# Kernel tuning notes

Hardware: AMD Instinct MI355X
Metric: run time of the kernel (lower is better)

The kernel has to match this reference:

```python
import jax, jax.numpy as jnp
import numpy as np

H = 16  # num_heads

def setup_inputs() -> dict:
    key = jax.random.key(0)
    ks = jax.random.split(key, 5)
    C = 1024
    x = jax.random.normal(ks[0], (4, 2048, C), dtype=jnp.float32)
    # torch nn.Linear params: weight (out, in), bias (out,)
    qkv_w = jax.random.normal(ks[1], (3 * C, C), dtype=jnp.float32) * (C ** -0.5)
    qkv_b = jnp.zeros((3 * C,), dtype=jnp.float32)
    proj_w = jax.random.normal(ks[2], (C, C), dtype=jnp.float32) * (C ** -0.5)
    proj_b = jnp.zeros((C,), dtype=jnp.float32)
    return {"x": x, "qkv_w": qkv_w, "qkv_b": qkv_b, "proj_w": proj_w, "proj_b": proj_b}

def reference(x, qkv_w, qkv_b, proj_w, proj_b):
    B, T, C = x.shape
    hd = C // H
    scale = hd ** -0.5
    qkv = x @ qkv_w.T + qkv_b                      # [B,T,3C]
    qkv = qkv.reshape(B, T, 3, H, hd)
    q, k, v = jnp.moveaxis(qkv, 2, 0)              # each [B,T,H,hd]
    q = q.transpose(0, 2, 1, 3)                    # [B,H,T,hd]
    k = k.transpose(0, 2, 1, 3)
    v = v.transpose(0, 2, 1, 3)
    attn = jnp.einsum('bhqd,bhkd->bhqk', q, k) * scale
    attn = jax.nn.softmax(attn, axis=-1)           # dropout is identity at eval
    out = jnp.einsum('bhqk,bhkd->bhqd', attn, v)   # [B,H,T,hd]
    out = out.transpose(0, 2, 1, 3).reshape(B, T, C)
    return out @ proj_w.T + proj_b
```

## Files before the change

kernel.cpp:

```cpp
#include <hip/hip_runtime.h>


typedef _Float16 f16x8 __attribute__((ext_vector_type(8)));
typedef _Float16 f16x4 __attribute__((ext_vector_type(4)));
typedef __fp16 h16x2 __attribute__((ext_vector_type(2)));
typedef float f32x4 __attribute__((ext_vector_type(4)));

__device__ __forceinline__ uint4 cvt8h(const float* p) {
    float4 a = *(const float4*)p, b = *(const float4*)(p + 4);
    union { _Float16 h[8]; uint4 u; } t;
    t.h[0] = (_Float16)a.x; t.h[1] = (_Float16)a.y;
    t.h[2] = (_Float16)a.z; t.h[3] = (_Float16)a.w;
    t.h[4] = (_Float16)b.x; t.h[5] = (_Float16)b.y;
    t.h[6] = (_Float16)b.z; t.h[7] = (_Float16)b.w;
    return t.u;
}

__device__ __forceinline__ void dma16(const _Float16* g, _Float16* l) {
    __builtin_amdgcn_global_load_lds(
        (const __attribute__((address_space(1))) unsigned int*)g,
        (__attribute__((address_space(3))) unsigned int*)l, 16, 0, 0);
}

__global__ __launch_bounds__(256) void cvt_fp16(
    const float* __restrict__ x, const float* __restrict__ w1,
    const float* __restrict__ w2,
    _Float16* __restrict__ xh, _Float16* __restrict__ w1h,
    _Float16* __restrict__ w2h)
{
    const int g = blockIdx.x * 256 + threadIdx.x;
    const float* src; _Float16* dst; int off;
    if (g < 1048576)      { src = x;  dst = xh;  off = g; }
    else if (g < 1441792) { src = w1; dst = w1h; off = g - 1048576; }
    else                  { src = w2; dst = w2h; off = g - 1441792; }
    const size_t e = (size_t)off * 8;
    *(uint4*)(dst + e) = cvt8h(src + e);
}

__global__ __launch_bounds__(256) void qkv_gemm(
    const _Float16* __restrict__ X, const _Float16* __restrict__ W,
    const float* __restrict__ Bias,
    _Float16* __restrict__ qws, _Float16* __restrict__ kws,
    _Float16* __restrict__ vtws)
{
    __shared__ _Float16 sA[128 * 32];
    __shared__ _Float16 sB[128 * 32];
    const int tid = threadIdx.x;
    const int wave = tid >> 6, lane = tid & 63;
    const int wm = (wave >> 1) * 64, wn = (wave & 1) * 64;
    const int lr = lane & 15, lq = lane >> 4;
    const int m0 = blockIdx.y * 128, n0 = blockIdx.x * 128;
    const int s = n0 >> 10;

    const int drow = wave * 16 + (lane >> 2);
    const int dcol = (lane & 3) * 8;
    _Float16* ldsA = sA + wave * 512;
    _Float16* ldsB = sB + wave * 512;
    const _Float16* gA = X + (size_t)(m0 + drow) * 1024 + dcol;
    const _Float16* gB = W + (size_t)(n0 + drow) * 1024 + dcol;

    f32x4 acc[4][4] = {};

    for (int k0 = 0; k0 < 1024; k0 += 32) {
        dma16(gA + k0, ldsA);
        dma16(gA + (size_t)64 * 1024 + k0, ldsA + 2048);
        dma16(gB + k0, ldsB);
        dma16(gB + (size_t)64 * 1024 + k0, ldsB + 2048);
        __syncthreads();
        f16x8 af[4], bf[4];
        #pragma unroll
        for (int i = 0; i < 4; ++i) {
            af[i] = *(const f16x8*)&sA[(wm + i * 16 + lr) * 32 + lq * 8];
            bf[i] = *(const f16x8*)&sB[(wn + i * 16 + lr) * 32 + lq * 8];
        }
        #pragma unroll
        for (int mi = 0; mi < 4; ++mi)
            #pragma unroll
            for (int ni = 0; ni < 4; ++ni)
                acc[mi][ni] = __builtin_amdgcn_mfma_f32_16x16x32_f16(
                    af[mi], bf[ni], acc[mi][ni], 0, 0, 0);
        __syncthreads();
    }

    #pragma unroll
    for (int mi = 0; mi < 4; ++mi) {
        #pragma unroll
        for (int ni = 0; ni < 4; ++ni) {
            const int n = n0 + wn + ni * 16 + lr;
            const float bv = Bias[n];
            const int h = (n >> 6) & 15, d = n & 63;
            const int mbase = m0 + wm + mi * 16 + lq * 4;
            const int b = mbase >> 11, t0 = mbase & 2047;
            const int bh = b * 16 + h;
            if (s == 0) {
                #pragma unroll
                for (int r = 0; r < 4; ++r)
                    qws[((size_t)bh * 2048 + t0 + r) * 64 + d] =
                        (_Float16)((acc[mi][ni][r] + bv) * 0.18033688f);
            } else if (s == 1) {
                #pragma unroll
                for (int r = 0; r < 4; ++r)
                    kws[((size_t)bh * 2048 + t0 + r) * 64 + d] =
                        (_Float16)(acc[mi][ni][r] + bv);
            } else {
                f16x4 pk;
                #pragma unroll
                for (int r = 0; r < 4; ++r) pk[r] = (_Float16)(acc[mi][ni][r] + bv);
                *(f16x4*)&vtws[((size_t)bh * 64 + d) * 2048 + t0] = pk;
            }
        }
    }
}

__global__ __launch_bounds__(256, 4) void attn_kernel(
    const _Float16* __restrict__ qws,
    const _Float16* __restrict__ kws,
    const _Float16* __restrict__ vtws,
    _Float16* __restrict__ ows)
{
    __shared__ _Float16 sK[64][72];
    __shared__ _Float16 sV[64][72];
    const int bid = blockIdx.x;
    const int bh = (bid & 7) * 8 + ((bid >> 3) & 7);
    const int qb = bid >> 6;
    const int tid = threadIdx.x, wave = tid >> 6, lane = tid & 63;
    const int lr = lane & 15, lq = lane >> 4;

    const _Float16* gq = qws + ((size_t)bh * 2048 + qb * 128) * 64;
    f16x8 aQ[2][2];
    #pragma unroll
    for (int mb = 0; mb < 2; ++mb)
        #pragma unroll
        for (int ks = 0; ks < 2; ++ks)
            aQ[mb][ks] = *(const f16x8*)&gq[(wave * 32 + mb * 16 + lr) * 64 + ks * 32 + lq * 8];

    f32x4 o[2][4] = {};
    float l_loc[2] = {};

    for (int kt = 0; kt < 32; ++kt) {
        const _Float16* gk = kws + ((size_t)bh * 2048 + kt * 64) * 64;
        const _Float16* gv = vtws + (size_t)bh * 64 * 2048 + kt * 64;
        __syncthreads();
        for (int i = tid; i < 512; i += 256) {
            const int row = i >> 3, c = (i & 7) * 8;
            *(uint4*)&sK[row][c] = *(const uint4*)&gk[row * 64 + c];
            *(uint4*)&sV[row][c] = *(const uint4*)&gv[(size_t)row * 2048 + c];
        }
        __syncthreads();

        f16x8 bK[2][4];
        #pragma unroll
        for (int ks = 0; ks < 2; ++ks)
            #pragma unroll
            for (int nb = 0; nb < 4; ++nb)
                bK[ks][nb] = *(const f16x8*)&sK[nb * 16 + lr][ks * 32 + lq * 8];
        f32x4 st[4][2] = {};
        __builtin_amdgcn_s_setprio(1);
        #pragma unroll
        for (int nb = 0; nb < 4; ++nb)
            #pragma unroll
            for (int mb = 0; mb < 2; ++mb) {
                st[nb][mb] = __builtin_amdgcn_mfma_f32_16x16x32_f16(
                    bK[0][nb], aQ[mb][0], st[nb][mb], 0, 0, 0);
                st[nb][mb] = __builtin_amdgcn_mfma_f32_16x16x32_f16(
                    bK[1][nb], aQ[mb][1], st[nb][mb], 0, 0, 0);
            }
        __builtin_amdgcn_s_setprio(0);

        f16x4 pB16[4][2];
        #pragma unroll
        for (int nb = 0; nb < 4; ++nb)
            #pragma unroll
            for (int mb = 0; mb < 2; ++mb) {
                float e0 = exp2f(st[nb][mb][0]);
                float e1 = exp2f(st[nb][mb][1]);
                float e2 = exp2f(st[nb][mb][2]);
                float e3 = exp2f(st[nb][mb][3]);
                l_loc[mb] += (e0 + e1) + (e2 + e3);
                union { h16x2 v2[2]; f16x4 v4; } u;
                u.v2[0] = __builtin_amdgcn_cvt_pkrtz(e0, e1);
                u.v2[1] = __builtin_amdgcn_cvt_pkrtz(e2, e3);
                pB16[nb][mb] = u.v4;
            }

        __builtin_amdgcn_s_setprio(1);
        #pragma unroll
        for (int nb = 0; nb < 4; ++nb) {
            f16x4 vA16[4];
            #pragma unroll
            for (int db = 0; db < 4; ++db)
                vA16[db] = *(const f16x4*)&sV[db * 16 + lr][nb * 16 + lq * 4];
            #pragma unroll
            for (int mb = 0; mb < 2; ++mb)
                #pragma unroll
                for (int db = 0; db < 4; ++db)
                    o[mb][db] = __builtin_amdgcn_mfma_f32_16x16x16f16(
                        vA16[db], pB16[nb][mb], o[mb][db], 0, 0, 0);
        }
        __builtin_amdgcn_s_setprio(0);
    }

    const int b = bh >> 4, h = bh & 15;
    #pragma unroll
    for (int mb = 0; mb < 2; ++mb) {
        float l = l_loc[mb];
        l += __shfl_xor(l, 16, 64);
        l += __shfl_xor(l, 32, 64);
        const float linv = 1.0f / l;
        const int t = qb * 128 + wave * 32 + mb * 16 + lr;
        #pragma unroll
        for (int db = 0; db < 4; ++db) {
            f16x4 pk;
            #pragma unroll
            for (int reg = 0; reg < 4; ++reg)
                pk[reg] = (_Float16)(o[mb][db][reg] * linv);
            *(f16x4*)&ows[((size_t)(b * 2048 + t)) * 1024 + h * 64 + db * 16 + lq * 4] = pk;
        }
    }
}

__global__ __launch_bounds__(256) void proj_gemm(
    const _Float16* __restrict__ A, const _Float16* __restrict__ W,
    const float* __restrict__ Bias, float* __restrict__ out)
{
    __shared__ _Float16 sA[128 * 32];
    __shared__ _Float16 sB[128 * 32];
    const int tid = threadIdx.x;
    const int wave = tid >> 6, lane = tid & 63;
    const int wm = (wave >> 1) * 64, wn = (wave & 1) * 64;
    const int lr = lane & 15, lq = lane >> 4;
    const int m0 = blockIdx.y * 128, n0 = blockIdx.x * 128;

    const int drow = wave * 16 + (lane >> 2);
    const int dcol = (lane & 3) * 8;
    _Float16* ldsA = sA + wave * 512;
    _Float16* ldsB = sB + wave * 512;
    const _Float16* gA = A + (size_t)(m0 + drow) * 1024 + dcol;
    const _Float16* gB = W + (size_t)(n0 + drow) * 1024 + dcol;

    f32x4 acc[4][4] = {};

    for (int k0 = 0; k0 < 1024; k0 += 32) {
        dma16(gA + k0, ldsA);
        dma16(gA + (size_t)64 * 1024 + k0, ldsA + 2048);
        dma16(gB + k0, ldsB);
        dma16(gB + (size_t)64 * 1024 + k0, ldsB + 2048);
        __syncthreads();
        f16x8 af[4], bf[4];
        #pragma unroll
        for (int i = 0; i < 4; ++i) {
            af[i] = *(const f16x8*)&sA[(wm + i * 16 + lr) * 32 + lq * 8];
            bf[i] = *(const f16x8*)&sB[(wn + i * 16 + lr) * 32 + lq * 8];
        }
        #pragma unroll
        for (int mi = 0; mi < 4; ++mi)
            #pragma unroll
            for (int ni = 0; ni < 4; ++ni)
                acc[mi][ni] = __builtin_amdgcn_mfma_f32_16x16x32_f16(
                    af[mi], bf[ni], acc[mi][ni], 0, 0, 0);
        __syncthreads();
    }

    #pragma unroll
    for (int mi = 0; mi < 4; ++mi) {
        #pragma unroll
        for (int ni = 0; ni < 4; ++ni) {
            const int n = n0 + wn + ni * 16 + lr;
            const float bv = Bias[n];
            #pragma unroll
            for (int r = 0; r < 4; ++r) {
                const int m = m0 + wm + mi * 16 + lq * 4 + r;
                out[(size_t)m * 1024 + n] = acc[mi][ni][r] + bv;
            }
        }
    }
}

extern "C" void kernel_launch(void* const* d_in, const int* in_sizes, int n_in,
                              void* d_out, int out_size, void* d_ws, size_t ws_size,
                              hipStream_t stream) {
    const float* x      = (const float*)d_in[0];
    const float* qkv_w  = (const float*)d_in[1];
    const float* qkv_b  = (const float*)d_in[2];
    const float* proj_w = (const float*)d_in[3];
    const float* proj_b = (const float*)d_in[4];
    float* out = (float*)d_out;

    char* ws = (char*)d_ws;
    _Float16* qws  = (_Float16*)(ws);
    _Float16* kws  = (_Float16*)(ws + 16777216u);
    _Float16* vtws = (_Float16*)(ws + 33554432u);
    _Float16* ows  = (_Float16*)(ws + 50331648u);
    _Float16* Xh   = (_Float16*)(ws + 67108864u);
    _Float16* Wqh  = (_Float16*)(ws + 83886080u);
    _Float16* Wph  = (_Float16*)(ws + 90177536u);

    cvt_fp16<<<dim3(6144), 256, 0, stream>>>(x, qkv_w, proj_w, Xh, Wqh, Wph);
    qkv_gemm<<<dim3(24, 64), 256, 0, stream>>>(Xh, Wqh, qkv_b, qws, kws, vtws);
    attn_kernel<<<dim3(1024), 256, 0, stream>>>(qws, kws, vtws, ows);
    proj_gemm<<<dim3(8, 64), 256, 0, stream>>>(ows, Wph, proj_b, out);
}
```

Before: 306.5 us.

## Load K/V tiles via global_load_lds DMA with XOR-swizzled LDS layout

Replaces the register-staged global-to-LDS copy of K and V^T tiles in the attention kernel with direct global_load_lds transfers of 16 bytes per lane. Because the DMA writes contiguous rows, the LDS padding is removed and replaced by an XOR swizzle on the column index, with the read side adjusted to match. The intent is to cut VGPR traffic and instruction count for the tile copies while avoiding bank conflicts without padding. It depends on the swizzle mapping being consistent between the writers and readers, and the loop still synchronizes around each load.

```diff
diff --git a/kernel.cpp b/kernel.cpp
--- a/kernel.cpp
+++ b/kernel.cpp
@@ -118,8 +118,8 @@
     const _Float16* __restrict__ vtws,
     _Float16* __restrict__ ows)
 {
-    __shared__ _Float16 sK[64][72];
-    __shared__ _Float16 sV[64][72];
+    __shared__ _Float16 sK[64][64];
+    __shared__ _Float16 sV[64][64];
     const int bid = blockIdx.x;
     const int bh = (bid & 7) * 8 + ((bid >> 3) & 7);
     const int qb = bid >> 6;
@@ -134,26 +134,36 @@
         for (int ks = 0; ks < 2; ++ks)
             aQ[mb][ks] = *(const f16x8*)&gq[(wave * 32 + mb * 16 + lr) * 64 + ks * 32 + lq * 8];
 
+    const int l8 = lane >> 3;
+    const int swzcol = (((lane & 7) * 16) ^ (l8 << 4)) >> 1;
+    const int krow = wave * 8 + l8;
+    const _Float16* gk = kws + (size_t)bh * 2048 * 64 + (size_t)krow * 64 + swzcol;
+    const _Float16* gv = vtws + (size_t)bh * 64 * 2048 + (size_t)krow * 2048 + swzcol;
+    _Float16* dK = &sK[0][0] + wave * 512;
+    _Float16* dV = &sV[0][0] + wave * 512;
+
+    const int r7 = lr & 7;
+    const int cidx0 = ((lq * 16) ^ (r7 << 4)) >> 1;
+    const int cidx1 = ((64 + lq * 16) ^ (r7 << 4)) >> 1;
+
     f32x4 o[2][4] = {};
     float l_loc[2] = {};
 
     for (int kt = 0; kt < 32; ++kt) {
-        const _Float16* gk = kws + ((size_t)bh * 2048 + kt * 64) * 64;
-        const _Float16* gv = vtws + (size_t)bh * 64 * 2048 + kt * 64;
-        __syncthreads();
-        for (int i = tid; i < 512; i += 256) {
-            const int row = i >> 3, c = (i & 7) * 8;
-            *(uint4*)&sK[row][c] = *(const uint4*)&gk[row * 64 + c];
-            *(uint4*)&sV[row][c] = *(const uint4*)&gv[(size_t)row * 2048 + c];
-        }
+        __syncthreads();
+        dma16(gk,                     dK);
+        dma16(gk + 32 * 64,           dK + 2048);
+        dma16(gv,                     dV);
+        dma16(gv + (size_t)32 * 2048, dV + 2048);
+        gk += 4096; gv += 64;
         __syncthreads();
 
         f16x8 bK[2][4];
         #pragma unroll
-        for (int ks = 0; ks < 2; ++ks)
-            #pragma unroll
-            for (int nb = 0; nb < 4; ++nb)
-                bK[ks][nb] = *(const f16x8*)&sK[nb * 16 + lr][ks * 32 + lq * 8];
+        for (int nb = 0; nb < 4; ++nb) {
+            bK[0][nb] = *(const f16x8*)&sK[nb * 16 + lr][cidx0];
+            bK[1][nb] = *(const f16x8*)&sK[nb * 16 + lr][cidx1];
+        }
         f32x4 st[4][2] = {};
         __builtin_amdgcn_s_setprio(1);
         #pragma unroll
@@ -189,7 +199,8 @@
             f16x4 vA16[4];
             #pragma unroll
             for (int db = 0; db < 4; ++db)
-                vA16[db] = *(const f16x4*)&sV[db * 16 + lr][nb * 16 + lq * 4];
+                vA16[db] = *(const f16x4*)&sV[db * 16 + lr]
+                    [((nb * 32 + lq * 8) ^ (r7 << 4)) >> 1];
             #pragma unroll
             for (int mb = 0; mb < 2; ++mb)
                 #pragma unroll
```

New measurement: 302.0 us. Within noise of the previous version (-1.5%).
